# Performance work log

Hardware: AMD Instinct MI355X
Metric: run time of the kernel (lower is better)

The kernel has to match this reference:

```python
import jax, jax.numpy as jnp
import numpy as np

K = 20
EPS = 1e-5


def _bn(h, g, b, axes):
    m = jnp.mean(h, axes, keepdims=True)
    v = jnp.var(h, axes, keepdims=True)
    return (h - m) * jax.lax.rsqrt(v + EPS) * g + b


def _edge_feat(h):
    # h: [B,N,D] -> edge features [B,N,K,2D] = concat(central, neighbor-central)
    sq = jnp.sum(h * h, -1)
    # negative squared pairwise distance (larger = closer)
    adj = 2.0 * jnp.einsum('bnd,bmd->bnm', h, h) - sq[:, :, None] - sq[:, None, :]
    idx = jax.lax.top_k(adj, K)[1]  # [B,N,K] nearest (incl. self)
    nbr = jax.vmap(lambda hb, ib: hb[ib])(h, idx)  # [B,N,K,D]
    ctr = jnp.broadcast_to(h[:, :, None, :], nbr.shape)
    return jnp.concatenate([ctr, nbr - ctr], -1)


def _edge_layer(h, W, b, g, be):
    # 1x1 conv over edge features, relu THEN batchnorm (matches torch: bn(relu(conv))), max over K
    ef = _edge_feat(h)
    z = jax.nn.relu(jnp.einsum('bnkc,oc->bnko', ef, W) + b)
    z = _bn(z, g, be, (0, 1, 2))
    return jnp.max(z, axis=2)  # [B,N,O]


def _c1d(h, W, b):
    return jnp.einsum('bcl,oc->bol', h, W) + b[None, :, None]


def _bnc(h, g, b):
    m = jnp.mean(h, (0, 2), keepdims=True)
    v = jnp.var(h, (0, 2), keepdims=True)
    return (h - m) * jax.lax.rsqrt(v + EPS) * g[None, :, None] + b[None, :, None]


def _forward(x, rand_grid, W1, b1, g1, be1, W2, b2, g2, be2, W3, b3, g3, be3,
             W4, b4, g4, be4, W5, b5, g5, be5, lW, lb, lg, lbe,
             dW1, db1, dg1, dbe1, dW2, db2, dg2, dbe2, dW3, db3, dg3, dbe3, dW4, db4):
    pts = jnp.transpose(x, (0, 2, 1))  # [B,N,3]
    x1 = _edge_layer(pts, W1, b1, g1, be1)   # [B,N,64]
    x2 = _edge_layer(x1, W2, b2, g2, be2)    # [B,N,64]
    x3 = _edge_layer(x2, W3, b3, g3, be3)    # [B,N,64]
    x4 = _edge_layer(x3, W4, b4, g4, be4)    # [B,N,128]
    cat = jnp.concatenate([x1, x2, x3, x4], -1)  # [B,N,320]
    z = jax.nn.relu(jnp.einsum('bnc,oc->bno', cat, W5) + b5)
    z = _bn(z, g5, be5, (0, 1))
    glob = jnp.max(z, axis=1)  # [B,1024]
    lat = glob @ lW.T + lb
    lat = jax.nn.relu(_bn(lat, lg, lbe, (0,)))  # [B,1024]
    B, C = lat.shape
    P = rand_grid.shape[2]
    y = jnp.concatenate([rand_grid, jnp.broadcast_to(lat[:, :, None], (B, C, P))], axis=1)  # [B,1026,P]
    h = jax.nn.relu(_bnc(_c1d(y, dW1, db1), dg1, dbe1))
    h = jax.nn.relu(_bnc(_c1d(h, dW2, db2), dg2, dbe2))
    h = jax.nn.relu(_bnc(_c1d(h, dW3, db3), dg3, dbe3))
    return jnp.tanh(_c1d(h, dW4, db4))  # [B,3,P]


def setup_inputs() -> dict:
    key = jax.random.key(0)
    ks = iter(jax.random.split(key, 64))
    B, N, BOT = 8, 2048, 1024
    D = BOT + 2  # 1026
    f32 = jnp.float32

    def w(o, c):
        return jax.random.normal(next(ks), (o, c), dtype=f32) * 0.05

    def bnp(c):
        return jnp.ones((c,), f32), jnp.zeros((c,), f32)

    inp = {
        'x': jax.random.normal(next(ks), (B, 3, N), dtype=f32),
        'rand_grid': jax.random.uniform(next(ks), (B, 2, N), dtype=f32),
    }
    enc = [(64, 6), (64, 128), (64, 128), (128, 128), (1024, 320)]
    for i, (o, c) in enumerate(enc, 1):
        inp[f'W{i}'] = w(o, c)
        inp[f'b{i}'] = jnp.zeros((o,), f32)
        inp[f'g{i}'], inp[f'be{i}'] = bnp(o)
    inp['lW'] = w(BOT, 1024)
    inp['lb'] = jnp.zeros((BOT,), f32)
    inp['lg'], inp['lbe'] = bnp(BOT)
    dec = [(D, D), (D // 2, D), (D // 4, D // 2), (3, D // 4)]
    for i, (o, c) in enumerate(dec, 1):
        inp[f'dW{i}'] = w(o, c)
        inp[f'db{i}'] = jnp.zeros((o,), f32)
        if i < 4:
            inp[f'dg{i}'], inp[f'dbe{i}'] = bnp(o)
    return inp


def reference(x, rand_grid, W1, b1, g1, be1, W2, b2, g2, be2, W3, b3, g3, be3,
              W4, b4, g4, be4, W5, b5, g5, be5, lW, lb, lg, lbe,
              dW1, db1, dg1, dbe1, dW2, db2, dg2, dbe2, dW3, db3, dg3, dbe3, dW4, db4):
    return _forward(x, rand_grid, W1, b1, g1, be1, W2, b2, g2, be2, W3, b3, g3, be3,
                    W4, b4, g4, be4, W5, b5, g5, be5, lW, lb, lg, lbe,
                    dW1, db1, dg1, dbe1, dW2, db2, dg2, dbe2, dW3, db3, dg3, dbe3, dW4, db4)
```

## Files before the change

kernel.cpp:

```cpp
#include <hip/hip_runtime.h>
#include <math.h>

constexpr int NB = 8;
constexpr int NN = 2048;
constexpr int NK = 20;
constexpr int NP = 2048;


__global__ void transpose_x_kernel(const float* __restrict__ x, float* __restrict__ pts) {
  int gid = blockIdx.x * 256 + threadIdx.x;
  if (gid >= NB * NN * 3) return;
  int c = gid % 3;
  int n = (gid / 3) % NN;
  int b = gid / (3 * NN);
  pts[gid] = x[(b * 3 + c) * NN + n];
}

__global__ void transpose_mat_ld(const float* __restrict__ src, float* __restrict__ dst, int R,
                                 int C, int ldd) {
  __shared__ float tile[32][33];
  int c0 = blockIdx.x * 32, r0 = blockIdx.y * 32;
  int tx = threadIdx.x & 31, ty = threadIdx.x >> 5;
  for (int i = ty; i < 32; i += 8) {
    int r = r0 + i, c = c0 + tx;
    tile[i][tx] = (r < R && c < C) ? src[(size_t)r * C + c] : 0.f;
  }
  __syncthreads();
  for (int i = ty; i < 32; i += 8) {
    int c = c0 + i, r = r0 + tx;
    if (r < R && c < C) dst[(size_t)c * ldd + r] = tile[tx][i];
  }
}

__global__ void knn3_fused_kernel(const float* __restrict__ pts, int* __restrict__ idx) {
  __shared__ float sm[3][NN];
  int t = threadIdx.x;
  int l = t & 63, w = t >> 6;
  int gb = blockIdx.x;
  int b = gb >> 9;
  int n0 = (gb & 511) * 4;
  const float* base = pts + (size_t)b * NN * 3;
  for (int e = t; e < NN * 3; e += 256) {
    int col = e / 3, d = e - col * 3;
    sm[d][col] = base[e];
  }
  __syncthreads();
  int n = n0 + w;
  float c0 = sm[0][n], c1 = sm[1][n], c2 = sm[2][n];
  float v[32];
#pragma unroll
  for (int j = 0; j < 32; j++) {
    int col = j * 64 + l;
    float d0 = c0 - sm[0][col];
    float d1 = c1 - sm[1][col];
    float d2 = c2 - sm[2][col];
    float acc = 0.f;
    acc = fmaf(d0, d0, acc);
    acc = fmaf(d1, d1, acc);
    acc = fmaf(d2, d2, acc);
    v[j] = -acc;
  }
  int mykm = 0;
  for (int k = 0; k < NK; k++) {
    float bv = v[0];
    int bj = 0;
#pragma unroll
    for (int j = 1; j < 32; j++) {
      if (v[j] > bv) { bv = v[j]; bj = j; }
    }
    int gm = bj * 64 + l;
#pragma unroll
    for (int off = 32; off; off >>= 1) {
      float ov = __shfl_xor(bv, off, 64);
      int om = __shfl_xor(gm, off, 64);
      if (ov > bv || (ov == bv && om < gm)) { bv = ov; gm = om; }
    }
    if (l == k) mykm = gm;
    int jb = gm >> 6, lb = gm & 63;
#pragma unroll
    for (int j = 0; j < 32; j++)
      if (j == jb && l == lb) v[j] = -3e38f;
  }
  if (l < NK) idx[((size_t)(b * NN + n)) * NK + l] = mykm;
}

__global__ __launch_bounds__(256, 2) void knn_dist128_kernel(const float* __restrict__ h, int ld,
                                                             int coff, int b0,
                                                             float* __restrict__ dmat) {
  __shared__ float sc[16][132];
  __shared__ float sr[16][128];
  int t = threadIdx.x;
  int c0 = blockIdx.x * 128, r0 = blockIdx.y * 128;
  int bz = blockIdx.z;
  const float* rows = h + ((size_t)(b0 + bz) * NN) * ld + coff;
  int arow = t >> 1, ac = (t & 1) * 8;
  int tx = t & 15, ty = t >> 4;
  float acc[8][8] = {};
  float rA[8], rB[8];

  auto gload = [&](int d0) {
    const float* pc = &rows[(size_t)(c0 + arow) * ld + d0 + ac];
    float4 a0 = *(const float4*)pc;
    float4 a1 = *(const float4*)(pc + 4);
    rA[0] = a0.x; rA[1] = a0.y; rA[2] = a0.z; rA[3] = a0.w;
    rA[4] = a1.x; rA[5] = a1.y; rA[6] = a1.z; rA[7] = a1.w;
    const float* pr = &rows[(size_t)(r0 + arow) * ld + d0 + ac];
    float4 b0 = *(const float4*)pr;
    float4 b1 = *(const float4*)(pr + 4);
    rB[0] = b0.x; rB[1] = b0.y; rB[2] = b0.z; rB[3] = b0.w;
    rB[4] = b1.x; rB[5] = b1.y; rB[6] = b1.z; rB[7] = b1.w;
  };
  auto ldswrite = [&]() {
#pragma unroll
    for (int j = 0; j < 8; j++) {
      sc[ac + j][arow] = rA[j];
      sr[ac + j][arow] = rB[j];
    }
  };

  gload(0);
  for (int ks = 0; ks < 4; ks++) {
    __syncthreads();
    ldswrite();
    __syncthreads();
    if (ks + 1 < 4) gload((ks + 1) * 16);
#pragma unroll
    for (int d = 0; d < 16; d++) {
      float4 a0 = *(const float4*)&sc[d][ty * 4];
      float4 a1 = *(const float4*)&sc[d][64 + ty * 4];
      float4 b0 = *(const float4*)&sr[d][tx * 4];
      float4 b1 = *(const float4*)&sr[d][64 + tx * 4];
      float av[8] = {a0.x, a0.y, a0.z, a0.w, a1.x, a1.y, a1.z, a1.w};
      float bv[8] = {b0.x, b0.y, b0.z, b0.w, b1.x, b1.y, b1.z, b1.w};
#pragma unroll
      for (int i = 0; i < 8; i++)
#pragma unroll
        for (int j = 0; j < 8; j++) {
          float dd = av[i] - bv[j];
          acc[i][j] = fmaf(dd, dd, acc[i][j]);
        }
    }
  }
#pragma unroll
  for (int i = 0; i < 8; i++) {
    int c = c0 + (i < 4 ? ty * 4 + i : 64 + ty * 4 + (i - 4));
    float* dst = &dmat[((size_t)bz * NN + c) * NN + r0];
    float4 q0, q1;
    q0.x = -acc[i][0]; q0.y = -acc[i][1]; q0.z = -acc[i][2]; q0.w = -acc[i][3];
    q1.x = -acc[i][4]; q1.y = -acc[i][5]; q1.z = -acc[i][6]; q1.w = -acc[i][7];
    *(float4*)&dst[tx * 4] = q0;
    *(float4*)&dst[64 + tx * 4] = q1;
  }
}

__global__ void knn_topk_kernel(const float* __restrict__ dmat, int b0, int* __restrict__ idx) {
  int t = threadIdx.x;
  int l = t & 63;
  int w = t >> 6;
  int gr = blockIdx.x * 4 + w;
  int bz = gr >> 11;
  int n = gr & 2047;
  const float* row = dmat + ((size_t)bz * NN + n) * NN;
  float v[32];
#pragma unroll
  for (int j = 0; j < 32; j++) v[j] = row[j * 64 + l];
  int mykm = 0;
  for (int k = 0; k < NK; k++) {
    float bv = v[0];
    int bj = 0;
#pragma unroll
    for (int j = 1; j < 32; j++) {
      if (v[j] > bv) { bv = v[j]; bj = j; }
    }
    int gm = bj * 64 + l;
#pragma unroll
    for (int off = 32; off; off >>= 1) {
      float ov = __shfl_xor(bv, off, 64);
      int om = __shfl_xor(gm, off, 64);
      if (ov > bv || (ov == bv && om < gm)) { bv = ov; gm = om; }
    }
    if (l == k) mykm = gm;
    int jb = gm >> 6, lb = gm & 63;
#pragma unroll
    for (int j = 0; j < 32; j++)
      if (j == jb && l == lb) v[j] = -3e38f;
  }
  if (l < NK) idx[((size_t)((b0 + bz) * NN + n)) * NK + l] = mykm;
}

__global__ void weff_kernel(const float* __restrict__ W, int O, int D, float* __restrict__ Weff) {
  int i = blockIdx.x * 256 + threadIdx.x;
  if (i >= 2 * O * D) return;
  int o = i / D, d = i - o * D;
  float v;
  if (o < O) v = W[(size_t)o * 2 * D + d] - W[(size_t)o * 2 * D + D + d];
  else v = W[(size_t)(o - O) * 2 * D + D + d];
  Weff[i] = v;
}

template <int M2, int D>
__global__ __launch_bounds__(256, 4) void pgemm_kernel(const float* __restrict__ h, int ld,
                                                       int coff, const float* __restrict__ Weff,
                                                       const float* __restrict__ bias,
                                                       float* __restrict__ P) {
  constexpr int O = M2 / 2;
  constexpr int GRP = 256 / M2;
  constexpr int NR = 8 / GRP;
  __shared__ float sh[8][D == 3 ? 4 : 68];
  int t = threadIdx.x;
  int n0 = blockIdx.x * 8;
  const float* base = h + coff;
  if constexpr (D == 64) {
    if (t < 128) {
      int r = t >> 4, q = (t & 15) * 4;
      *(float4*)&sh[r][q] = *(const float4*)&base[(size_t)(n0 + r) * ld + q];
    }
  } else {
    if (t < 24) {
      int r = t / 3, c = t - r * 3;
      sh[r][c] = base[(size_t)(n0 + r) * ld + c];
    }
  }
  __syncthreads();
  int o = t % M2;
  int gi = t / M2;
  float acc[NR];
  float bz = (o < O) ? bias[o] : 0.f;
#pragma unroll
  for (int j = 0; j < NR; j++) acc[j] = bz;
  const float* wr = Weff + (size_t)o * D;
  if constexpr (D == 64) {
#pragma unroll
    for (int d4 = 0; d4 < 16; d4++) {
      float4 w4 = *(const float4*)&wr[d4 * 4];
#pragma unroll
      for (int j = 0; j < NR; j++) {
        float4 e4 = *(const float4*)&sh[gi * NR + j][d4 * 4];
        acc[j] = fmaf(w4.x, e4.x, acc[j]);
        acc[j] = fmaf(w4.y, e4.y, acc[j]);
        acc[j] = fmaf(w4.z, e4.z, acc[j]);
        acc[j] = fmaf(w4.w, e4.w, acc[j]);
      }
    }
  } else {
    float w0 = wr[0], w1 = wr[1], w2 = wr[2];
#pragma unroll
    for (int j = 0; j < NR; j++) {
      int r = gi * NR + j;
      acc[j] = fmaf(w0, sh[r][0], fmaf(w1, sh[r][1], fmaf(w2, sh[r][2], acc[j])));
    }
  }
#pragma unroll
  for (int j = 0; j < NR; j++)
    P[(size_t)(n0 + gi * NR + j) * M2 + o] = acc[j];
}

template <int O>
__global__ __launch_bounds__(256, 8) void combine_kernel(const float* __restrict__ P,
                                                         const int* __restrict__ idx,
                                                         float* __restrict__ zmax,
                                                         float* __restrict__ zmin,
                                                         float* __restrict__ psum,
                                                         float* __restrict__ psq) {
  constexpr int CPB = 256 / O;
  constexpr int M2 = 2 * O;
  __shared__ int sidx[CPB * NK];
  int t = threadIdx.x;
  int bn0 = blockIdx.x * CPB;
  if (t < CPB * NK) sidx[t] = idx[(size_t)bn0 * NK + t];
  __syncthreads();
  int g = t / O, o = t % O;
  int bn = bn0 + g;
  int b = bn >> 11;
  float p1 = P[(size_t)bn * M2 + o];
  const float* P2 = P + (size_t)b * NN * M2 + O + o;
  float s = 0.f, sq = 0.f, mx = -3e38f, mn = 3e38f;
#pragma unroll
  for (int k = 0; k < NK; k++) {
    int nb = sidx[g * NK + k];
    float z = fmaxf(p1 + P2[(size_t)nb * M2], 0.f);
    s += z;
    sq = fmaf(z, z, sq);
    mx = fmaxf(mx, z);
    mn = fminf(mn, z);
  }
  zmax[(size_t)bn * O + o] = mx;
  zmin[(size_t)bn * O + o] = mn;
  psum[(size_t)o * (NB * NN) + bn] = s;
  psq[(size_t)o * (NB * NN) + bn] = sq;
}

__global__ void edge_reduce_kernel(const float* __restrict__ psum, const float* __restrict__ psq,
                                   const float* __restrict__ g, const float* __restrict__ be,
                                   float* __restrict__ scale, float* __restrict__ shift,
                                   double inv_n) {
  int o = blockIdx.x, t = threadIdx.x;
  double s = 0.0, q = 0.0;
  const float* ps = psum + (size_t)o * (NB * NN);
  const float* pq = psq + (size_t)o * (NB * NN);
  for (int i = t; i < NB * NN; i += 256) { s += (double)ps[i]; q += (double)pq[i]; }
  __shared__ double rs[256], rq[256];
  rs[t] = s; rq[t] = q;
  __syncthreads();
  for (int st = 128; st; st >>= 1) {
    if (t < st) { rs[t] += rs[t + st]; rq[t] += rq[t + st]; }
    __syncthreads();
  }
  if (t == 0) {
    double mean = rs[0] * inv_n;
    double var = rq[0] * inv_n - mean * mean;
    double r = 1.0 / sqrt(var + 1e-5);
    double sc = (double)g[o] * r;
    scale[o] = (float)sc;
    shift[o] = (float)((double)be[o] - mean * sc);
  }
}

__global__ void edge_affine_kernel(const float* __restrict__ zmax, const float* __restrict__ zmin,
                                   const float* __restrict__ scale, const float* __restrict__ shift,
                                   float* __restrict__ cat, int O, int coff_out) {
  int gid = blockIdx.x * 256 + threadIdx.x;
  int o = gid % O;
  int bn = gid / O;
  float sc = scale[o];
  float v = (sc >= 0.f) ? zmax[gid] : zmin[gid];
  cat[(size_t)bn * 320 + coff_out + o] = fmaf(sc, v, shift[o]);
}

__global__ __launch_bounds__(256, 2) void gemm5_64_kernel(const float* __restrict__ cat,
                                                          const float* __restrict__ W5t,
                                                          const float* __restrict__ b5,
                                                          float* __restrict__ z5) {
  __shared__ float sA[32][64];
  __shared__ float sB[32][128];
  int t = threadIdx.x;
  int r0 = blockIdx.x * 64, m0 = blockIdx.y * 128;
  int arow = t & 63, ach = (t >> 6) * 8;
  int blr = t >> 4, blc = (t & 15) * 8;
  int tx = t & 15, ty = t >> 4;
  float acc[4][8] = {};
  float rA[8], rB[16];

  auto gload = [&](int c0) {
    const float* pa = &cat[(size_t)(r0 + arow) * 320 + c0 + ach];
    float4 a0 = *(const float4*)pa;
    float4 a1 = *(const float4*)(pa + 4);
    rA[0] = a0.x; rA[1] = a0.y; rA[2] = a0.z; rA[3] = a0.w;
    rA[4] = a1.x; rA[5] = a1.y; rA[6] = a1.z; rA[7] = a1.w;
    const float* pb = &W5t[(size_t)(c0 + blr) * 1024 + m0 + blc];
    float4 b0 = *(const float4*)pb;
    float4 b1 = *(const float4*)(pb + 4);
    rB[0] = b0.x; rB[1] = b0.y; rB[2] = b0.z; rB[3] = b0.w;
    rB[4] = b1.x; rB[5] = b1.y; rB[6] = b1.z; rB[7] = b1.w;
    const float* pb2 = &W5t[(size_t)(c0 + 16 + blr) * 1024 + m0 + blc];
    float4 c4 = *(const float4*)pb2;
    float4 c5 = *(const float4*)(pb2 + 4);
    rB[8] = c4.x; rB[9] = c4.y; rB[10] = c4.z; rB[11] = c4.w;
    rB[12] = c5.x; rB[13] = c5.y; rB[14] = c5.z; rB[15] = c5.w;
  };
  auto ldswrite = [&]() {
#pragma unroll
    for (int j = 0; j < 8; j++) sA[ach + j][arow] = rA[j];
    float4 w0, w1;
    w0.x = rB[0]; w0.y = rB[1]; w0.z = rB[2]; w0.w = rB[3];
    w1.x = rB[4]; w1.y = rB[5]; w1.z = rB[6]; w1.w = rB[7];
    *(float4*)&sB[blr][blc] = w0;
    *(float4*)&sB[blr][blc + 4] = w1;
    w0.x = rB[8]; w0.y = rB[9]; w0.z = rB[10]; w0.w = rB[11];
    w1.x = rB[12]; w1.y = rB[13]; w1.z = rB[14]; w1.w = rB[15];
    *(float4*)&sB[16 + blr][blc] = w0;
    *(float4*)&sB[16 + blr][blc + 4] = w1;
  };

  gload(0);
  for (int kt = 0; kt < 10; kt++) {
    __syncthreads();
    ldswrite();
    __syncthreads();
    if (kt + 1 < 10) gload((kt + 1) * 32);
#pragma unroll
    for (int c = 0; c < 32; c++) {
      float4 a0 = *(const float4*)&sA[c][ty * 4];
      float4 b0 = *(const float4*)&sB[c][tx * 4];
      float4 b1 = *(const float4*)&sB[c][64 + tx * 4];
      float av[4] = {a0.x, a0.y, a0.z, a0.w};
      float bv[8] = {b0.x, b0.y, b0.z, b0.w, b1.x, b1.y, b1.z, b1.w};
#pragma unroll
      for (int i = 0; i < 4; i++)
#pragma unroll
        for (int j = 0; j < 8; j++) acc[i][j] = fmaf(av[i], bv[j], acc[i][j]);
    }
  }
  float bj[8];
#pragma unroll
  for (int j = 0; j < 8; j++)
    bj[j] = b5[m0 + (j < 4 ? tx * 4 + j : 64 + tx * 4 + (j - 4))];
#pragma unroll
  for (int i = 0; i < 4; i++) {
    int r = r0 + ty * 4 + i;
    float* dst = &z5[(size_t)r * 1024 + m0];
    float4 q0, q1;
    q0.x = fmaxf(acc[i][0] + bj[0], 0.f);
    q0.y = fmaxf(acc[i][1] + bj[1], 0.f);
    q0.z = fmaxf(acc[i][2] + bj[2], 0.f);
    q0.w = fmaxf(acc[i][3] + bj[3], 0.f);
    q1.x = fmaxf(acc[i][4] + bj[4], 0.f);
    q1.y = fmaxf(acc[i][5] + bj[5], 0.f);
    q1.z = fmaxf(acc[i][6] + bj[6], 0.f);
    q1.w = fmaxf(acc[i][7] + bj[7], 0.f);
    *(float4*)&dst[tx * 4] = q0;
    *(float4*)&dst[64 + tx * 4] = q1;
  }
}

__global__ void stats5_kernel(const float* __restrict__ z5, double* __restrict__ psum5,
                              double* __restrict__ psq5, float* __restrict__ pmax5,
                              float* __restrict__ pmin5) {
  int j = blockIdx.x, t = threadIdx.x;
  int row0 = j * 64;
  double s0 = 0, s1 = 0, s2 = 0, s3 = 0, q0 = 0, q1 = 0, q2 = 0, q3 = 0;
  float4 mx = {-3e38f, -3e38f, -3e38f, -3e38f}, mn = {3e38f, 3e38f, 3e38f, 3e38f};
  for (int r = 0; r < 64; r++) {
    float4 v = *(const float4*)&z5[(size_t)(row0 + r) * 1024 + t * 4];
    s0 += v.x; s1 += v.y; s2 += v.z; s3 += v.w;
    q0 += (double)v.x * v.x; q1 += (double)v.y * v.y;
    q2 += (double)v.z * v.z; q3 += (double)v.w * v.w;
    mx.x = fmaxf(mx.x, v.x); mx.y = fmaxf(mx.y, v.y); mx.z = fmaxf(mx.z, v.z); mx.w = fmaxf(mx.w, v.w);
    mn.x = fminf(mn.x, v.x); mn.y = fminf(mn.y, v.y); mn.z = fminf(mn.z, v.z); mn.w = fminf(mn.w, v.w);
  }
  size_t base = (size_t)j * 1024 + t * 4;
  psum5[base + 0] = s0; psum5[base + 1] = s1; psum5[base + 2] = s2; psum5[base + 3] = s3;
  psq5[base + 0] = q0; psq5[base + 1] = q1; psq5[base + 2] = q2; psq5[base + 3] = q3;
  *(float4*)&pmax5[base] = mx;
  *(float4*)&pmin5[base] = mn;
}

__global__ void reduce5_glob_kernel(const double* __restrict__ psum5, const double* __restrict__ psq5,
                                    const float* __restrict__ pmax5, const float* __restrict__ pmin5,
                                    const float* __restrict__ g5, const float* __restrict__ be5,
                                    float* __restrict__ glob) {
  int o = blockIdx.x * 256 + threadIdx.x;
  double s = 0.0, q = 0.0;
  for (int j = 0; j < 256; j++) {
    s += psum5[(size_t)j * 1024 + o];
    q += psq5[(size_t)j * 1024 + o];
  }
  double mean = s * (1.0 / 16384.0);
  double var = q * (1.0 / 16384.0) - mean * mean;
  double r = 1.0 / sqrt(var + 1e-5);
  double scd = (double)g5[o] * r;
  float sc = (float)scd;
  float sh = (float)((double)be5[o] - mean * scd);
  for (int b = 0; b < 8; b++) {
    float m;
    if (sc >= 0.f) {
      m = -3e38f;
      for (int jj = 0; jj < 32; jj++) m = fmaxf(m, pmax5[(size_t)(b * 32 + jj) * 1024 + o]);
    } else {
      m = 3e38f;
      for (int jj = 0; jj < 32; jj++) m = fminf(m, pmin5[(size_t)(b * 32 + jj) * 1024 + o]);
    }
    glob[b * 1024 + o] = fmaf(sc, m, sh);
  }
}

__global__ void fc_kernel(const float* __restrict__ in, const float* __restrict__ Wt, int ld,
                          int coff, const float* __restrict__ bias, float* __restrict__ out,
                          int Ci, int Co) {
  __shared__ float sin_[1024];
  __shared__ float red[8][32];
  int b = blockIdx.x, t = threadIdx.x;
  for (int e = t; e < Ci; e += 256) sin_[e] = in[(size_t)b * Ci + e];
  __syncthreads();
  int o = blockIdx.y * 32 + (t & 31);
  int cg = t >> 5;
  int cn = Ci / 8;
  float p = 0.f;
  if (o < Co) {
    for (int c = cg * cn; c < (cg + 1) * cn; c++)
      p = fmaf(Wt[(size_t)(c + coff) * ld + o], sin_[c], p);
  }
  red[cg][t & 31] = p;
  __syncthreads();
  if (cg == 0 && o < Co) {
    float s = red[0][t] + red[1][t] + red[2][t] + red[3][t] + red[4][t] + red[5][t] + red[6][t] +
              red[7][t];
    out[(size_t)b * Co + o] = s + bias[o];
  }
}

__global__ void lat_bn_kernel(const float* __restrict__ latp, const float* __restrict__ lg,
                              const float* __restrict__ lbe, float* __restrict__ lat) {
  int o = blockIdx.x * 256 + threadIdx.x;
  float v[8];
  double s = 0.0, q = 0.0;
  for (int b = 0; b < 8; b++) {
    v[b] = latp[b * 1024 + o];
    s += (double)v[b];
    q += (double)v[b] * (double)v[b];
  }
  double mean = s * 0.125;
  double var = q * 0.125 - mean * mean;
  double r = 1.0 / sqrt(var + 1e-5);
  double gd = (double)lg[o], bd = (double)lbe[o];
  for (int b = 0; b < 8; b++) {
    float z = (float)(((double)v[b] - mean) * r * gd + bd);
    lat[b * 1024 + o] = fmaxf(z, 0.f);
  }
}

__global__ void dec1_z_kernel(const float* __restrict__ rg, const float* __restrict__ dW1t,
                              const float* __restrict__ u, float* __restrict__ z1) {
  int bo = blockIdx.x;
  int b = bo / 1026;
  int o = bo - b * 1026;
  int t = threadIdx.x;
  float w0 = dW1t[o], w1 = dW1t[1026 + o], ub = u[bo];
  const float4* r0 = (const float4*)(rg + (size_t)b * 2 * NP);
  const float4* r1 = (const float4*)(rg + (size_t)b * 2 * NP + NP);
  float4* zr = (float4*)(z1 + (size_t)bo * NP);
  for (int i = t; i < NP / 4; i += 256) {
    float4 a = r0[i], c = r1[i], rr;
    rr.x = fmaf(w0, a.x, fmaf(w1, c.x, ub));
    rr.y = fmaf(w0, a.y, fmaf(w1, c.y, ub));
    rr.z = fmaf(w0, a.z, fmaf(w1, c.z, ub));
    rr.w = fmaf(w0, a.w, fmaf(w1, c.w, ub));
    zr[i] = rr;
  }
}

__global__ void dstats_kernel(const float* __restrict__ z, int C, const float* __restrict__ g,
                              const float* __restrict__ be, float* __restrict__ scale,
                              float* __restrict__ shift) {
  int o = blockIdx.x, t = threadIdx.x;
  double s = 0.0, q = 0.0;
  for (int b = 0; b < 8; b++) {
    const float4* row = (const float4*)(z + ((size_t)b * C + o) * NP);
    for (int i = t; i < NP / 4; i += 256) {
      float4 v = row[i];
      s += (double)v.x + (double)v.y + (double)v.z + (double)v.w;
      q += (double)v.x * v.x + (double)v.y * v.y + (double)v.z * v.z + (double)v.w * v.w;
    }
  }
  __shared__ double rs[256], rq[256];
  rs[t] = s; rq[t] = q;
  __syncthreads();
  for (int st = 128; st; st >>= 1) {
    if (t < st) { rs[t] += rs[t + st]; rq[t] += rq[t + st]; }
    __syncthreads();
  }
  if (t == 0) {
    double inv = 1.0 / (8.0 * NP);
    double mean = rs[0] * inv;
    double var = rq[0] * inv - mean * mean;
    double r = 1.0 / sqrt(var + 1e-5);
    double sc = (double)g[o] * r;
    scale[o] = (float)sc;
    shift[o] = (float)((double)be[o] - mean * sc);
  }
}

template <int NMT>
__global__ __launch_bounds__(256, 2) void dec_gemm64s_kernel(
    const float* __restrict__ zin, const float* __restrict__ Wt, int ldA,
    const float* __restrict__ bias, const float* __restrict__ scale,
    const float* __restrict__ shift, float* __restrict__ zout, int Ci, int Co) {
  __shared__ float sA[32][64];
  __shared__ float sB[32][128];
  int bid = blockIdx.x;
  int gl = bid & 7;
  int q = bid >> 3;
  int gh = q / NMT;
  int mt = q - gh * NMT;
  int g = gl + (gh << 3);
  int pt = g & 15;
  int b = g >> 4;
  int m0 = mt * 64, p0 = pt * 128;
  int t = threadIdx.x;
  int lr = t >> 4, lcA = (t & 15) * 4, lcB = (t & 15) * 8;
  int tx = t & 15, ty = t >> 4;
  int numK = (Ci + 31) >> 5;
  float acc[4][8] = {};
  float rA[8], rB[16];

  auto gloadhalf = [&](int c, float* ra, float* rb) {
#pragma unroll
    for (int j = 0; j < 4; j++) ra[j] = 0.f;
#pragma unroll
    for (int j = 0; j < 8; j++) rb[j] = 0.f;
    if (c < Ci) {
      int mb = m0 + lcA;
      if (mb + 4 <= Co) {
        float4 a0 = *(const float4*)&Wt[(size_t)c * ldA + mb];
        ra[0] = a0.x; ra[1] = a0.y; ra[2] = a0.z; ra[3] = a0.w;
      } else {
#pragma unroll
        for (int j = 0; j < 4; j++)
          if (mb + j < Co) ra[j] = Wt[(size_t)c * ldA + mb + j];
      }
      float sc = scale[c], sh = shift[c];
      const float* src = &zin[((size_t)b * Ci + c) * NP + p0 + lcB];
      float4 z0 = *(const float4*)src;
      float4 z1 = *(const float4*)(src + 4);
      rb[0] = fmaxf(fmaf(sc, z0.x, sh), 0.f);
      rb[1] = fmaxf(fmaf(sc, z0.y, sh), 0.f);
      rb[2] = fmaxf(fmaf(sc, z0.z, sh), 0.f);
      rb[3] = fmaxf(fmaf(sc, z0.w, sh), 0.f);
      rb[4] = fmaxf(fmaf(sc, z1.x, sh), 0.f);
      rb[5] = fmaxf(fmaf(sc, z1.y, sh), 0.f);
      rb[6] = fmaxf(fmaf(sc, z1.z, sh), 0.f);
      rb[7] = fmaxf(fmaf(sc, z1.w, sh), 0.f);
    }
  };
  auto gload = [&](int kt) {
    gloadhalf(kt * 32 + lr, rA, rB);
    gloadhalf(kt * 32 + 16 + lr, rA + 4, rB + 8);
  };
  auto ldswrite = [&]() {
    float4 v0;
    v0.x = rA[0]; v0.y = rA[1]; v0.z = rA[2]; v0.w = rA[3];
    *(float4*)&sA[lr][lcA] = v0;
    v0.x = rA[4]; v0.y = rA[5]; v0.z = rA[6]; v0.w = rA[7];
    *(float4*)&sA[16 + lr][lcA] = v0;
    float4 w0, w1;
    w0.x = rB[0]; w0.y = rB[1]; w0.z = rB[2]; w0.w = rB[3];
    w1.x = rB[4]; w1.y = rB[5]; w1.z = rB[6]; w1.w = rB[7];
    *(float4*)&sB[lr][lcB] = w0;
    *(float4*)&sB[lr][lcB + 4] = w1;
    w0.x = rB[8]; w0.y = rB[9]; w0.z = rB[10]; w0.w = rB[11];
    w1.x = rB[12]; w1.y = rB[13]; w1.z = rB[14]; w1.w = rB[15];
    *(float4*)&sB[16 + lr][lcB] = w0;
    *(float4*)&sB[16 + lr][lcB + 4] = w1;
  };

  gload(0);
  for (int kt = 0; kt < numK; kt++) {
    __syncthreads();
    ldswrite();
    __syncthreads();
    if (kt + 1 < numK) gload(kt + 1);
#pragma unroll
    for (int c = 0; c < 32; c++) {
      float4 a0 = *(const float4*)&sA[c][ty * 4];
      float4 b0 = *(const float4*)&sB[c][tx * 4];
      float4 b1 = *(const float4*)&sB[c][64 + tx * 4];
      float av[4] = {a0.x, a0.y, a0.z, a0.w};
      float bv[8] = {b0.x, b0.y, b0.z, b0.w, b1.x, b1.y, b1.z, b1.w};
#pragma unroll
      for (int i = 0; i < 4; i++)
#pragma unroll
        for (int j = 0; j < 8; j++) acc[i][j] = fmaf(av[i], bv[j], acc[i][j]);
    }
  }
#pragma unroll
  for (int i = 0; i < 4; i++) {
    int m = m0 + ty * 4 + i;
    if (m < Co) {
      float bv = bias[m];
      float* dst = &zout[((size_t)b * Co + m) * NP + p0];
      float4 q0, q1;
      q0.x = acc[i][0] + bv; q0.y = acc[i][1] + bv;
      q0.z = acc[i][2] + bv; q0.w = acc[i][3] + bv;
      q1.x = acc[i][4] + bv; q1.y = acc[i][5] + bv;
      q1.z = acc[i][6] + bv; q1.w = acc[i][7] + bv;
      *(float4*)&dst[tx * 4] = q0;
      *(float4*)&dst[64 + tx * 4] = q1;
    }
  }
}

__global__ void dec_final_kernel(const float* __restrict__ z3, const float* __restrict__ dW4,
                                 const float* __restrict__ db4, const float* __restrict__ scale,
                                 const float* __restrict__ shift, float* __restrict__ out) {
  __shared__ float w4[3 * 256];
  __shared__ float sc[256], sh[256];
  __shared__ float red[4][64][3];
  int b = blockIdx.x, pc = blockIdx.y, t = threadIdx.x;
  for (int e = t; e < 768; e += 256) w4[e] = dW4[e];
  sc[t] = scale[t];
  sh[t] = shift[t];
  __syncthreads();
  int tp = t & 63, tc = t >> 6;
  int p = pc * 64 + tp;
  float a0 = 0.f, a1 = 0.f, a2 = 0.f;
  for (int c = tc * 64; c < tc * 64 + 64; c++) {
    float hv = fmaxf(fmaf(sc[c], z3[((size_t)(b * 256 + c)) * NP + p], sh[c]), 0.f);
    a0 = fmaf(w4[c], hv, a0);
    a1 = fmaf(w4[256 + c], hv, a1);
    a2 = fmaf(w4[512 + c], hv, a2);
  }
  red[tc][tp][0] = a0;
  red[tc][tp][1] = a1;
  red[tc][tp][2] = a2;
  __syncthreads();
  if (tc == 0) {
    a0 = red[0][tp][0] + red[1][tp][0] + red[2][tp][0] + red[3][tp][0];
    a1 = red[0][tp][1] + red[1][tp][1] + red[2][tp][1] + red[3][tp][1];
    a2 = red[0][tp][2] + red[1][tp][2] + red[2][tp][2] + red[3][tp][2];
    out[((size_t)b * 3 + 0) * NP + p] = tanhf(a0 + db4[0]);
    out[((size_t)b * 3 + 1) * NP + p] = tanhf(a1 + db4[1]);
    out[((size_t)b * 3 + 2) * NP + p] = tanhf(a2 + db4[2]);
  }
}


extern "C" void kernel_launch(void* const* d_in, const int* in_sizes, int n_in, void* d_out,
                              int out_size, void* d_ws, size_t ws_size, hipStream_t stream) {
  const float* x = (const float*)d_in[0];
  const float* rg = (const float*)d_in[1];
  const float* W1 = (const float*)d_in[2];
  const float* b1 = (const float*)d_in[3];
  const float* g1 = (const float*)d_in[4];
  const float* be1 = (const float*)d_in[5];
  const float* W2 = (const float*)d_in[6];
  const float* b2 = (const float*)d_in[7];
  const float* g2 = (const float*)d_in[8];
  const float* be2 = (const float*)d_in[9];
  const float* W3 = (const float*)d_in[10];
  const float* b3 = (const float*)d_in[11];
  const float* g3 = (const float*)d_in[12];
  const float* be3 = (const float*)d_in[13];
  const float* W4 = (const float*)d_in[14];
  const float* b4 = (const float*)d_in[15];
  const float* g4 = (const float*)d_in[16];
  const float* be4 = (const float*)d_in[17];
  const float* W5 = (const float*)d_in[18];
  const float* b5 = (const float*)d_in[19];
  const float* g5 = (const float*)d_in[20];
  const float* be5 = (const float*)d_in[21];
  const float* lW = (const float*)d_in[22];
  const float* lb = (const float*)d_in[23];
  const float* lg = (const float*)d_in[24];
  const float* lbe = (const float*)d_in[25];
  const float* dW1 = (const float*)d_in[26];
  const float* db1 = (const float*)d_in[27];
  const float* dg1 = (const float*)d_in[28];
  const float* dbe1 = (const float*)d_in[29];
  const float* dW2 = (const float*)d_in[30];
  const float* db2 = (const float*)d_in[31];
  const float* dg2 = (const float*)d_in[32];
  const float* dbe2 = (const float*)d_in[33];
  const float* dW3 = (const float*)d_in[34];
  const float* db3 = (const float*)d_in[35];
  const float* dg3 = (const float*)d_in[36];
  const float* dbe3 = (const float*)d_in[37];
  const float* dW4 = (const float*)d_in[38];
  const float* db4 = (const float*)d_in[39];
  float* out = (float*)d_out;

  float* ws = (float*)d_ws;
  size_t off = 0;
  auto alloc = [&](size_t n) {
    size_t r = off;
    off += (n + 255) & ~(size_t)255;
    return r;
  };
  size_t f_pts = alloc((size_t)NB * NN * 3);
  size_t f_uA = alloc(13959168);
  size_t f_cat = f_uA;
  size_t f_idx = f_cat + 5242880;
  size_t f_zmax = f_idx + 327680;
  size_t f_zmin = f_zmax + 2097152;
  size_t f_psum = f_zmin + 2097152;
  size_t f_psq = f_psum + 2097152;
  size_t f_z2 = f_uA;
  size_t f_uB = alloc(16809984);
  size_t f_z5 = f_uB, f_z1 = f_uB;
  float* dmat = ws + f_uB;
  float* P = ws + f_uB;
  size_t f_uC = alloc(4194304);
  double* ps5_d = (double*)(ws + f_uC);
  double* pq5_d = ps5_d + 262144;
  size_t f_pM5 = f_uC + 2097152;
  size_t f_pm5 = f_pM5 + 262144;
  size_t f_z3 = f_uC;
  size_t f_weff = alloc(256 * 64);
  size_t f_W5t = alloc(320 * 1024);
  size_t f_lWt = alloc(1024 * 1024);
  size_t f_dW1t = alloc((size_t)1026 * 1026);
  size_t f_dW2t = alloc((size_t)1026 * 516);
  size_t f_dW3t = alloc(513 * 256);
  size_t f_scale = alloc(2048);
  size_t f_shift = alloc(2048);
  size_t f_glob = alloc(8 * 1024);
  size_t f_latp = alloc(8 * 1024);
  size_t f_lat = alloc(8 * 1024);
  size_t f_u = alloc(8 * 1026);
  (void)ws_size;
  (void)in_sizes;
  (void)n_in;
  (void)out_size;

  float* cat = ws + f_cat;
  int* idxp = (int*)(ws + f_idx);
  float* zmax = ws + f_zmax;
  float* zmin = ws + f_zmin;
  float* psumf = ws + f_psum;
  float* psqf = ws + f_psq;
  float* weff = ws + f_weff;
  float* scale = ws + f_scale;
  float* shift = ws + f_shift;
  const double invn_e = 1.0 / (double)(NB * NN * NK);

  transpose_x_kernel<<<192, 256, 0, stream>>>(x, ws + f_pts);
  transpose_mat_ld<<<dim3(10, 32), 256, 0, stream>>>(W5, ws + f_W5t, 1024, 320, 1024);
  transpose_mat_ld<<<dim3(32, 32), 256, 0, stream>>>(lW, ws + f_lWt, 1024, 1024, 1024);
  transpose_mat_ld<<<dim3(33, 33), 256, 0, stream>>>(dW1, ws + f_dW1t, 1026, 1026, 1026);
  transpose_mat_ld<<<dim3(33, 17), 256, 0, stream>>>(dW2, ws + f_dW2t, 513, 1026, 516);
  transpose_mat_ld<<<dim3(17, 8), 256, 0, stream>>>(dW3, ws + f_dW3t, 256, 513, 256);

  auto run_knn64 = [&](const float* h, int coff) {
    for (int bb0 = 0; bb0 < NB; bb0 += 4) {
      knn_dist128_kernel<<<dim3(16, 16, 4), 256, 0, stream>>>(h, 320, coff, bb0, dmat);
      knn_topk_kernel<<<2048, 256, 0, stream>>>(dmat, bb0, idxp);
    }
  };

  knn3_fused_kernel<<<NB * NN / 4, 256, 0, stream>>>(ws + f_pts, idxp);
  weff_kernel<<<2, 256, 0, stream>>>(W1, 64, 3, weff);
  pgemm_kernel<128, 3><<<2048, 256, 0, stream>>>(ws + f_pts, 3, 0, weff, b1, P);
  combine_kernel<64><<<4096, 256, 0, stream>>>(P, idxp, zmax, zmin, psumf, psqf);
  edge_reduce_kernel<<<64, 256, 0, stream>>>(psumf, psqf, g1, be1, scale, shift, invn_e);
  edge_affine_kernel<<<NB * NN * 64 / 256, 256, 0, stream>>>(zmax, zmin, scale, shift, cat, 64, 0);
  run_knn64(cat, 0);
  weff_kernel<<<32, 256, 0, stream>>>(W2, 64, 64, weff);
  pgemm_kernel<128, 64><<<2048, 256, 0, stream>>>(cat, 320, 0, weff, b2, P);
  combine_kernel<64><<<4096, 256, 0, stream>>>(P, idxp, zmax, zmin, psumf, psqf);
  edge_reduce_kernel<<<64, 256, 0, stream>>>(psumf, psqf, g2, be2, scale, shift, invn_e);
  edge_affine_kernel<<<NB * NN * 64 / 256, 256, 0, stream>>>(zmax, zmin, scale, shift, cat, 64, 64);
  run_knn64(cat, 64);
  weff_kernel<<<32, 256, 0, stream>>>(W3, 64, 64, weff);
  pgemm_kernel<128, 64><<<2048, 256, 0, stream>>>(cat, 320, 64, weff, b3, P);
  combine_kernel<64><<<4096, 256, 0, stream>>>(P, idxp, zmax, zmin, psumf, psqf);
  edge_reduce_kernel<<<64, 256, 0, stream>>>(psumf, psqf, g3, be3, scale, shift, invn_e);
  edge_affine_kernel<<<NB * NN * 64 / 256, 256, 0, stream>>>(zmax, zmin, scale, shift, cat, 64, 128);
  run_knn64(cat, 128);
  weff_kernel<<<64, 256, 0, stream>>>(W4, 128, 64, weff);
  pgemm_kernel<256, 64><<<2048, 256, 0, stream>>>(cat, 320, 128, weff, b4, P);
  combine_kernel<128><<<8192, 256, 0, stream>>>(P, idxp, zmax, zmin, psumf, psqf);
  edge_reduce_kernel<<<128, 256, 0, stream>>>(psumf, psqf, g4, be4, scale, shift, invn_e);
  edge_affine_kernel<<<NB * NN * 128 / 256, 256, 0, stream>>>(zmax, zmin, scale, shift, cat, 128, 192);

  gemm5_64_kernel<<<dim3(256, 8), 256, 0, stream>>>(cat, ws + f_W5t, b5, ws + f_z5);
  stats5_kernel<<<256, 256, 0, stream>>>(ws + f_z5, ps5_d, pq5_d, ws + f_pM5, ws + f_pm5);
  reduce5_glob_kernel<<<4, 256, 0, stream>>>(ps5_d, pq5_d, ws + f_pM5, ws + f_pm5, g5, be5,
                                             ws + f_glob);
  fc_kernel<<<dim3(8, 32), 256, 0, stream>>>(ws + f_glob, ws + f_lWt, 1024, 0, lb, ws + f_latp,
                                             1024, 1024);
  lat_bn_kernel<<<4, 256, 0, stream>>>(ws + f_latp, lg, lbe, ws + f_lat);
  fc_kernel<<<dim3(8, 33), 256, 0, stream>>>(ws + f_lat, ws + f_dW1t, 1026, 2, db1, ws + f_u, 1024,
                                             1026);
  dec1_z_kernel<<<8 * 1026, 256, 0, stream>>>(rg, ws + f_dW1t, ws + f_u, ws + f_z1);
  dstats_kernel<<<1026, 256, 0, stream>>>(ws + f_z1, 1026, dg1, dbe1, scale, shift);
  dec_gemm64s_kernel<9><<<9 * 128, 256, 0, stream>>>(ws + f_z1, ws + f_dW2t, 516, db2, scale,
                                                     shift, ws + f_z2, 1026, 513);
  dstats_kernel<<<513, 256, 0, stream>>>(ws + f_z2, 513, dg2, dbe2, scale, shift);
  dec_gemm64s_kernel<4><<<4 * 128, 256, 0, stream>>>(ws + f_z2, ws + f_dW3t, 256, db3, scale,
                                                     shift, ws + f_z3, 513, 256);
  dstats_kernel<<<256, 256, 0, stream>>>(ws + f_z3, 256, dg3, dbe3, scale, shift);
  dec_final_kernel<<<dim3(8, 32), 256, 0, stream>>>(ws + f_z3, dW4, db4, scale, shift, out);
}
```

Measured before the change: 1.829 ms.

## Fuse kNN distance computation with top-k selection for 64-dim edge layers

Replaces the two-pass kNN for the 64-channel edge layers with one kernel. The old path wrote a full pairwise distance matrix to global memory and then ran a separate top-k pass over it. The new kernel gives each wavefront one query point: it streams all candidate points through shared memory in 128-column tiles and keeps the 32 distances per lane in registers before doing the warp-level top-20. This removes the large distance-matrix round trip through memory and halves the launch count. In exchange it drops the 8x8 register tiling of the old distance GEMM, so each FMA needs more shared-memory reads, and every block rereads all candidate features. It also relies on a tie-break index remapping for the interleaved column layout.

```diff
diff --git a/kernel.cpp b/kernel.cpp
--- a/kernel.cpp
+++ b/kernel.cpp
@@ -84,86 +84,51 @@
   if (l < NK) idx[((size_t)(b * NN + n)) * NK + l] = mykm;
 }
 
-__global__ __launch_bounds__(256, 2) void knn_dist128_kernel(const float* __restrict__ h, int ld,
-                                                             int coff, int b0,
-                                                             float* __restrict__ dmat) {
-  __shared__ float sc[16][132];
-  __shared__ float sr[16][128];
+__global__ __launch_bounds__(1024) void knn64_fused_kernel(const float* __restrict__ h, int ld,
+                                                           int coff, int* __restrict__ idx) {
+  __shared__ float sft[64][128];
+  __shared__ float sctr[16][64];
   int t = threadIdx.x;
-  int c0 = blockIdx.x * 128, r0 = blockIdx.y * 128;
-  int bz = blockIdx.z;
-  const float* rows = h + ((size_t)(b0 + bz) * NN) * ld + coff;
-  int arow = t >> 1, ac = (t & 1) * 8;
-  int tx = t & 15, ty = t >> 4;
-  float acc[8][8] = {};
-  float rA[8], rB[8];
-
-  auto gload = [&](int d0) {
-    const float* pc = &rows[(size_t)(c0 + arow) * ld + d0 + ac];
-    float4 a0 = *(const float4*)pc;
-    float4 a1 = *(const float4*)(pc + 4);
-    rA[0] = a0.x; rA[1] = a0.y; rA[2] = a0.z; rA[3] = a0.w;
-    rA[4] = a1.x; rA[5] = a1.y; rA[6] = a1.z; rA[7] = a1.w;
-    const float* pr = &rows[(size_t)(r0 + arow) * ld + d0 + ac];
-    float4 b0 = *(const float4*)pr;
-    float4 b1 = *(const float4*)(pr + 4);
-    rB[0] = b0.x; rB[1] = b0.y; rB[2] = b0.z; rB[3] = b0.w;
-    rB[4] = b1.x; rB[5] = b1.y; rB[6] = b1.z; rB[7] = b1.w;
-  };
-  auto ldswrite = [&]() {
-#pragma unroll
-    for (int j = 0; j < 8; j++) {
-      sc[ac + j][arow] = rA[j];
-      sr[ac + j][arow] = rB[j];
-    }
-  };
-
-  gload(0);
-  for (int ks = 0; ks < 4; ks++) {
+  int l = t & 63, w = t >> 6;
+  int n0 = blockIdx.x * 16;
+  int b = blockIdx.y;
+  const float* rows = h + (size_t)b * NN * ld + coff;
+  {
+    int r = t >> 6, d = t & 63;
+    sctr[r][d] = rows[(size_t)(n0 + r) * ld + d];
+  }
+  int col_l = t >> 3;
+  int d0 = (t & 7) * 8;
+  float v[32];
+#pragma unroll
+  for (int ct = 0; ct < 16; ct++) {
     __syncthreads();
-    ldswrite();
+    {
+      const float* src = &rows[(size_t)(ct * 128 + col_l) * ld + d0];
+      float4 f0 = *(const float4*)src;
+      float4 f1 = *(const float4*)(src + 4);
+      sft[d0 + 0][col_l] = f0.x;
+      sft[d0 + 1][col_l] = f0.y;
+      sft[d0 + 2][col_l] = f0.z;
+      sft[d0 + 3][col_l] = f0.w;
+      sft[d0 + 4][col_l] = f1.x;
+      sft[d0 + 5][col_l] = f1.y;
+      sft[d0 + 6][col_l] = f1.z;
+      sft[d0 + 7][col_l] = f1.w;
+    }
     __syncthreads();
-    if (ks + 1 < 4) gload((ks + 1) * 16);
-#pragma unroll
-    for (int d = 0; d < 16; d++) {
-      float4 a0 = *(const float4*)&sc[d][ty * 4];
-      float4 a1 = *(const float4*)&sc[d][64 + ty * 4];
-      float4 b0 = *(const float4*)&sr[d][tx * 4];
-      float4 b1 = *(const float4*)&sr[d][64 + tx * 4];
-      float av[8] = {a0.x, a0.y, a0.z, a0.w, a1.x, a1.y, a1.z, a1.w};
-      float bv[8] = {b0.x, b0.y, b0.z, b0.w, b1.x, b1.y, b1.z, b1.w};
-#pragma unroll
-      for (int i = 0; i < 8; i++)
-#pragma unroll
-        for (int j = 0; j < 8; j++) {
-          float dd = av[i] - bv[j];
-          acc[i][j] = fmaf(dd, dd, acc[i][j]);
-        }
-    }
-  }
-#pragma unroll
-  for (int i = 0; i < 8; i++) {
-    int c = c0 + (i < 4 ? ty * 4 + i : 64 + ty * 4 + (i - 4));
-    float* dst = &dmat[((size_t)bz * NN + c) * NN + r0];
-    float4 q0, q1;
-    q0.x = -acc[i][0]; q0.y = -acc[i][1]; q0.z = -acc[i][2]; q0.w = -acc[i][3];
-    q1.x = -acc[i][4]; q1.y = -acc[i][5]; q1.z = -acc[i][6]; q1.w = -acc[i][7];
-    *(float4*)&dst[tx * 4] = q0;
-    *(float4*)&dst[64 + tx * 4] = q1;
-  }
-}
-
-__global__ void knn_topk_kernel(const float* __restrict__ dmat, int b0, int* __restrict__ idx) {
-  int t = threadIdx.x;
-  int l = t & 63;
-  int w = t >> 6;
-  int gr = blockIdx.x * 4 + w;
-  int bz = gr >> 11;
-  int n = gr & 2047;
-  const float* row = dmat + ((size_t)bz * NN + n) * NN;
-  float v[32];
-#pragma unroll
-  for (int j = 0; j < 32; j++) v[j] = row[j * 64 + l];
+    float a0 = 0.f, a1 = 0.f;
+#pragma unroll 8
+    for (int d = 0; d < 64; d++) {
+      float cd = sctr[w][d];
+      float2 f = *(const float2*)&sft[d][2 * l];
+      float e0 = cd - f.x, e1 = cd - f.y;
+      a0 = fmaf(e0, e0, a0);
+      a1 = fmaf(e1, e1, a1);
+    }
+    v[2 * ct] = -a0;
+    v[2 * ct + 1] = -a1;
+  }
   int mykm = 0;
   for (int k = 0; k < NK; k++) {
     float bv = v[0];
@@ -172,7 +137,7 @@
     for (int j = 1; j < 32; j++) {
       if (v[j] > bv) { bv = v[j]; bj = j; }
     }
-    int gm = bj * 64 + l;
+    int gm = ((bj >> 1) << 7) + 2 * l + (bj & 1);
 #pragma unroll
     for (int off = 32; off; off >>= 1) {
       float ov = __shfl_xor(bv, off, 64);
@@ -180,12 +145,14 @@
       if (ov > bv || (ov == bv && om < gm)) { bv = ov; gm = om; }
     }
     if (l == k) mykm = gm;
-    int jb = gm >> 6, lb = gm & 63;
+    int rem = gm & 127;
+    int jb = ((gm >> 7) << 1) + (rem & 1);
+    int lb = rem >> 1;
 #pragma unroll
     for (int j = 0; j < 32; j++)
       if (j == jb && l == lb) v[j] = -3e38f;
   }
-  if (l < NK) idx[((size_t)((b0 + bz) * NN + n)) * NK + l] = mykm;
+  if (l < NK) idx[((size_t)(b * NN + n0 + w)) * NK + l] = mykm;
 }
 
 __global__ void weff_kernel(const float* __restrict__ W, int O, int D, float* __restrict__ Weff) {
@@ -766,7 +733,6 @@
   size_t f_z2 = f_uA;
   size_t f_uB = alloc(16809984);
   size_t f_z5 = f_uB, f_z1 = f_uB;
-  float* dmat = ws + f_uB;
   float* P = ws + f_uB;
   size_t f_uC = alloc(4194304);
   double* ps5_d = (double*)(ws + f_uC);
@@ -809,32 +775,25 @@
   transpose_mat_ld<<<dim3(33, 17), 256, 0, stream>>>(dW2, ws + f_dW2t, 513, 1026, 516);
   transpose_mat_ld<<<dim3(17, 8), 256, 0, stream>>>(dW3, ws + f_dW3t, 256, 513, 256);
 
-  auto run_knn64 = [&](const float* h, int coff) {
-    for (int bb0 = 0; bb0 < NB; bb0 += 4) {
-      knn_dist128_kernel<<<dim3(16, 16, 4), 256, 0, stream>>>(h, 320, coff, bb0, dmat);
-      knn_topk_kernel<<<2048, 256, 0, stream>>>(dmat, bb0, idxp);
-    }
-  };
-
   knn3_fused_kernel<<<NB * NN / 4, 256, 0, stream>>>(ws + f_pts, idxp);
   weff_kernel<<<2, 256, 0, stream>>>(W1, 64, 3, weff);
   pgemm_kernel<128, 3><<<2048, 256, 0, stream>>>(ws + f_pts, 3, 0, weff, b1, P);
   combine_kernel<64><<<4096, 256, 0, stream>>>(P, idxp, zmax, zmin, psumf, psqf);
   edge_reduce_kernel<<<64, 256, 0, stream>>>(psumf, psqf, g1, be1, scale, shift, invn_e);
   edge_affine_kernel<<<NB * NN * 64 / 256, 256, 0, stream>>>(zmax, zmin, scale, shift, cat, 64, 0);
-  run_knn64(cat, 0);
+  knn64_fused_kernel<<<dim3(128, 8), 1024, 0, stream>>>(cat, 320, 0, idxp);
   weff_kernel<<<32, 256, 0, stream>>>(W2, 64, 64, weff);
   pgemm_kernel<128, 64><<<2048, 256, 0, stream>>>(cat, 320, 0, weff, b2, P);
   combine_kernel<64><<<4096, 256, 0, stream>>>(P, idxp, zmax, zmin, psumf, psqf);
   edge_reduce_kernel<<<64, 256, 0, stream>>>(psumf, psqf, g2, be2, scale, shift, invn_e);
   edge_affine_kernel<<<NB * NN * 64 / 256, 256, 0, stream>>>(zmax, zmin, scale, shift, cat, 64, 64);
-  run_knn64(cat, 64);
+  knn64_fused_kernel<<<dim3(128, 8), 1024, 0, stream>>>(cat, 320, 64, idxp);
   weff_kernel<<<32, 256, 0, stream>>>(W3, 64, 64, weff);
   pgemm_kernel<128, 64><<<2048, 256, 0, stream>>>(cat, 320, 64, weff, b3, P);
   combine_kernel<64><<<4096, 256, 0, stream>>>(P, idxp, zmax, zmin, psumf, psqf);
   edge_reduce_kernel<<<64, 256, 0, stream>>>(psumf, psqf, g3, be3, scale, shift, invn_e);
   edge_affine_kernel<<<NB * NN * 64 / 256, 256, 0, stream>>>(zmax, zmin, scale, shift, cat, 64, 128);
-  run_knn64(cat, 128);
+  knn64_fused_kernel<<<dim3(128, 8), 1024, 0, stream>>>(cat, 320, 128, idxp);
   weff_kernel<<<64, 256, 0, stream>>>(W4, 128, 64, weff);
   pgemm_kernel<256, 64><<<2048, 256, 0, stream>>>(cat, 320, 128, weff, b4, P);
   combine_kernel<128><<<8192, 256, 0, stream>>>(P, idxp, zmax, zmin, psumf, psqf);
```

Measured after the change: 1.908 ms. 4.3% more time.
